# Performance work log

Hardware: AMD Instinct MI355X
Metric: run time of the kernel (lower is better)

## Reference

```python
import jax, jax.numpy as jnp
import numpy as np

N_WIDTH = 8
N_ORDER = 2
N_ELEMENTS = 1024
N_NODES = N_ELEMENTS * N_ORDER + 1  # 2049
N_SAMPLES = 4096
X_MIN = 0.0
X_MAX = 1.0


def _ref_nodes():
    return np.linspace(-1.0, 1.0, N_ORDER + 1)


def _lagrange(x):
    # x: [I, K] -> [I, K, P]
    nodes = _ref_nodes()
    cols = []
    for j in range(N_ORDER + 1):
        p = jnp.ones_like(x)
        for m in range(N_ORDER + 1):
            if j != m:
                p = p * (x - nodes[m]) / (nodes[j] - nodes[m])
        cols.append(p)
    return jnp.stack(cols, axis=-1)


def _dlagrange(x):
    nodes = _ref_nodes()
    cols = []
    for j in range(N_ORDER + 1):
        y = jnp.zeros_like(x)
        for i in range(N_ORDER + 1):
            if i != j:
                k = jnp.ones_like(x) / (nodes[j] - nodes[i])
                for m in range(N_ORDER + 1):
                    if m != i and m != j:
                        k = k * (x - nodes[m]) / (nodes[j] - nodes[m])
                y = y + k
        cols.append(y)
    return jnp.stack(cols, axis=-1)


def _ddlagrange(x):
    nodes = _ref_nodes()
    cols = []
    for j in range(N_ORDER + 1):
        y = jnp.zeros_like(x)
        for i in range(N_ORDER + 1):
            if i != j:
                k_sum = jnp.zeros_like(x)
                for m in range(N_ORDER + 1):
                    if m != i and m != j:
                        k_prod = jnp.ones_like(x) / (nodes[j] - nodes[m])
                        for n in range(N_ORDER + 1):
                            if n != i and n != j and n != m:
                                k_prod = k_prod * (x - nodes[n]) / (nodes[j] - nodes[n])
                        k_sum = k_sum + k_prod
                y = y + (1.0 / (nodes[j] - nodes[i])) * k_sum
        cols.append(y)
    return jnp.stack(cols, axis=-1)


def setup_inputs() -> dict:
    key = jax.random.key(0)
    k1, k2 = jax.random.split(key)
    x = jax.random.uniform(k1, (N_SAMPLES,), dtype=jnp.float32)  # in [x_min, x_max)
    weight = jax.random.normal(k2, (N_WIDTH, N_NODES), dtype=jnp.float32) * 0.02
    return {"x": x, "weight": weight}


def reference(x, weight):
    # replicate 1-D input across width: [I] -> [I, K]
    x2 = jnp.repeat(x[:, None], N_WIDTH, axis=-1)
    x_shift = (N_NODES - 1) * (x2 - X_MIN) / (X_MAX - X_MIN)
    id_el = jnp.clip(jnp.floor(x_shift / N_ORDER), 0, N_ELEMENTS - 1)
    nodes_l = (id_el * N_ORDER).astype(jnp.int32)  # [I, K]
    nodes_lf = jax.lax.stop_gradient(nodes_l.astype(x_shift.dtype))
    # reference coord: (x_shift - 0.5*(l + r)) / (0.5*(r - l)) with r = l + n_order
    x_t = (x_shift - (nodes_lf + 0.5 * N_ORDER)) / (0.5 * N_ORDER)

    delta_x = 0.5 * N_ORDER * (X_MAX - X_MIN) / (N_NODES - 1)
    phi_loc = _lagrange(x_t)                       # [I, K, P]
    dphi_loc = _dlagrange(x_t) / delta_x
    ddphi_loc = _ddlagrange(x_t) / (delta_x * delta_x)

    I, K = x2.shape
    P = N_ORDER + 1
    idx = nodes_l[:, :, None] + jnp.arange(P)      # [I, K, P] global node ids
    ii = jnp.arange(I)[:, None, None]
    kk = jnp.arange(K)[None, :, None]
    phi_ikp = jnp.zeros((I, K, N_NODES), x2.dtype).at[ii, kk, idx].set(phi_loc)
    dphi_ikp = jnp.zeros((I, K, N_NODES), x2.dtype).at[ii, kk, idx].set(dphi_loc)
    ddphi_ikp = jnp.zeros((I, K, N_NODES), x2.dtype).at[ii, kk, idx].set(ddphi_loc)

    t_ik = jnp.einsum('kp,ikp->ik', weight, phi_ikp)
    dt_ik = jnp.einsum('kp,ikp->ik', weight, dphi_ikp)
    ddt_ik = jnp.einsum('kp,ikp->ik', weight, ddphi_ikp)
    return (t_ik, dt_ik, ddt_ik, phi_ikp, dphi_ikp, ddphi_ikp)
```

## Files before the change

### kernel.cpp

```cpp
#include <hip/hip_runtime.h>


#define KN_WIDTH    8
#define KN_ORDER    2
#define KN_ELEMENTS 1024
#define KN_NODES    2049
#define KN_SAMPLES  4096

__global__ __launch_bounds__(256)
void KANN_4578435137547_scatter(const float* __restrict__ x,
                                const float* __restrict__ w,
                                float* __restrict__ out) {
    int i = blockIdx.x * blockDim.x + threadIdx.x;
    if (i >= KN_SAMPLES) return;

    float xv = x[i];
    float x_shift = 2048.0f * xv;
    float fid = floorf(x_shift * 0.5f);
    fid = fminf(fmaxf(fid, 0.0f), (float)(KN_ELEMENTS - 1));
    int nodes_l = (int)fid * KN_ORDER;
    float x_t = x_shift - ((float)nodes_l + 1.0f);

    float phi0 = 0.5f * x_t * (x_t - 1.0f);
    float phi1 = 1.0f - x_t * x_t;
    float phi2 = 0.5f * x_t * (x_t + 1.0f);

    const float inv_dx  = 2048.0f;
    const float inv_dx2 = inv_dx * inv_dx;
    float dphi0 = (x_t - 0.5f) * inv_dx;
    float dphi1 = (-2.0f * x_t) * inv_dx;
    float dphi2 = (x_t + 0.5f) * inv_dx;
    float dd0 =  1.0f * inv_dx2;
    float dd1 = -2.0f * inv_dx2;
    float dd2 =  1.0f * inv_dx2;

    const long long off_dt  = (long long)KN_SAMPLES * KN_WIDTH;
    const long long off_phi = 3LL * KN_SAMPLES * KN_WIDTH;
    const long long sz_phi  = (long long)KN_SAMPLES * KN_WIDTH * KN_NODES;

#pragma unroll
    for (int k = 0; k < KN_WIDTH; ++k) {
        const float* wk = w + k * KN_NODES + nodes_l;
        float w0 = wk[0], w1 = wk[1], w2 = wk[2];
        float t   = w0 * phi0  + w1 * phi1  + w2 * phi2;
        float dt  = w0 * dphi0 + w1 * dphi1 + w2 * dphi2;
        float ddt = w0 * dd0   + w1 * dd1   + w2 * dd2;

        long long ik = (long long)i * KN_WIDTH + k;
        out[ik]              = t;
        out[off_dt + ik]     = dt;
        out[2 * off_dt + ik] = ddt;

        long long base = off_phi + ik * KN_NODES + nodes_l;
        out[base + 0] = phi0;
        out[base + 1] = phi1;
        out[base + 2] = phi2;
        out[base + sz_phi + 0] = dphi0;
        out[base + sz_phi + 1] = dphi1;
        out[base + sz_phi + 2] = dphi2;
        out[base + 2 * sz_phi + 0] = dd0;
        out[base + 2 * sz_phi + 1] = dd1;
        out[base + 2 * sz_phi + 2] = dd2;
    }
}

extern "C" void kernel_launch(void* const* d_in, const int* in_sizes, int n_in,
                              void* d_out, int out_size, void* d_ws, size_t ws_size,
                              hipStream_t stream) {
    const float* x = (const float*)d_in[0];
    const float* w = (const float*)d_in[1];
    float* out = (float*)d_out;

    hipMemsetAsync(out, 0, (size_t)out_size * sizeof(float), stream);

    const int block = 256;
    const int grid = (KN_SAMPLES + block - 1) / block;
    KANN_4578435137547_scatter<<<grid, block, 0, stream>>>(x, w, out);
}
```

Baseline: 158.3 us.

## Replace memset plus scatter with a fused dense float4 writer of basis tensors

Drops the full-output memset and the scattered per-sample stores. A small head kernel now computes t/dt/ddt per (sample, width) thread. A grid-stride body kernel writes each of the three dense basis tensors in one float4-vectorized pass, filling zeros or basis values directly. This turns two passes over roughly 800 MB (clear, then sparse scatter) into one coalesced write stream. The cost is an integer division and a coordinate recompute per float4, plus a slow path for float4s that straddle row boundaries.

```diff
diff --git a/kernel.cpp b/kernel.cpp
--- a/kernel.cpp
+++ b/kernel.cpp
@@ -2,65 +2,86 @@
 
 
 #define KN_WIDTH    8
-#define KN_ORDER    2
-#define KN_ELEMENTS 1024
 #define KN_NODES    2049
 #define KN_SAMPLES  4096
+#define KN_IK       (KN_SAMPLES * KN_WIDTH)
+#define KN_HEAD     (3 * KN_IK)
+#define KN_PHI_LEN  ((size_t)KN_IK * KN_NODES)
+
+__device__ __forceinline__ void kann_coord(float xv, int& nl, float& x_t) {
+    float xs  = 2048.0f * xv;
+    float fid = floorf(0.5f * xs);
+    fid = fminf(fmaxf(fid, 0.0f), 1023.0f);
+    nl  = 2 * (int)fid;
+    x_t = xs - ((float)nl + 1.0f);
+}
 
 __global__ __launch_bounds__(256)
-void KANN_4578435137547_scatter(const float* __restrict__ x,
-                                const float* __restrict__ w,
-                                float* __restrict__ out) {
-    int i = blockIdx.x * blockDim.x + threadIdx.x;
-    if (i >= KN_SAMPLES) return;
+void KANN_head(const float* __restrict__ x, const float* __restrict__ w,
+               float* __restrict__ out) {
+    int ik = blockIdx.x * 256 + threadIdx.x;
+    if (ik >= KN_IK) return;
+    int i = ik >> 3, k = ik & 7;
+    int nl; float x_t; kann_coord(x[i], nl, x_t);
+    float p0 = 0.5f * x_t * (x_t - 1.0f);
+    float p1 = 1.0f - x_t * x_t;
+    float p2 = 0.5f * x_t * (x_t + 1.0f);
+    const float s = 2048.0f, s2 = 2048.0f * 2048.0f;
+    const float* wk = w + k * KN_NODES + nl;
+    float w0 = wk[0], w1 = wk[1], w2 = wk[2];
+    out[ik]             = w0 * p0 + w1 * p1 + w2 * p2;
+    out[KN_IK + ik]     = (w0 * (x_t - 0.5f) - 2.0f * w1 * x_t + w2 * (x_t + 0.5f)) * s;
+    out[2 * KN_IK + ik] = (w0 - 2.0f * w1 + w2) * s2;
+}
 
-    float xv = x[i];
-    float x_shift = 2048.0f * xv;
-    float fid = floorf(x_shift * 0.5f);
-    fid = fminf(fmaxf(fid, 0.0f), (float)(KN_ELEMENTS - 1));
-    int nodes_l = (int)fid * KN_ORDER;
-    float x_t = x_shift - ((float)nodes_l + 1.0f);
+__global__ __launch_bounds__(256)
+void KANN_body(const float* __restrict__ x, float* __restrict__ out) {
+    const int y = blockIdx.y;
+    float* base = out + KN_HEAD + (size_t)y * KN_PHI_LEN;
+    const unsigned nf4 = (unsigned)(KN_PHI_LEN / 4);
+    const unsigned stride = gridDim.x * blockDim.x;
 
-    float phi0 = 0.5f * x_t * (x_t - 1.0f);
-    float phi1 = 1.0f - x_t * x_t;
-    float phi2 = 0.5f * x_t * (x_t + 1.0f);
+    for (unsigned f4 = blockIdx.x * blockDim.x + threadIdx.x; f4 < nf4; f4 += stride) {
+        unsigned e0   = f4 * 4u;
+        unsigned row  = e0 / KN_NODES;
+        unsigned col0 = e0 - row * KN_NODES;
+        float vv[4] = {0.0f, 0.0f, 0.0f, 0.0f};
 
-    const float inv_dx  = 2048.0f;
-    const float inv_dx2 = inv_dx * inv_dx;
-    float dphi0 = (x_t - 0.5f) * inv_dx;
-    float dphi1 = (-2.0f * x_t) * inv_dx;
-    float dphi2 = (x_t + 0.5f) * inv_dx;
-    float dd0 =  1.0f * inv_dx2;
-    float dd1 = -2.0f * inv_dx2;
-    float dd2 =  1.0f * inv_dx2;
-
-    const long long off_dt  = (long long)KN_SAMPLES * KN_WIDTH;
-    const long long off_phi = 3LL * KN_SAMPLES * KN_WIDTH;
-    const long long sz_phi  = (long long)KN_SAMPLES * KN_WIDTH * KN_NODES;
-
+        if (col0 < KN_NODES - 3) {
+            int i = (int)(row >> 3);
+            int nl; float x_t; kann_coord(x[i], nl, x_t);
+            int d0 = (int)col0 - nl;
+            if (d0 >= -3 && d0 <= 2) {
+                float b0, b1, b2;
+                if (y == 0)      { b0 = 0.5f * x_t * (x_t - 1.0f); b1 = 1.0f - x_t * x_t; b2 = 0.5f * x_t * (x_t + 1.0f); }
+                else if (y == 1) { b0 = (x_t - 0.5f) * 2048.0f; b1 = -4096.0f * x_t; b2 = (x_t + 0.5f) * 2048.0f; }
+                else             { b0 = 4194304.0f; b1 = -8388608.0f; b2 = 4194304.0f; }
 #pragma unroll
-    for (int k = 0; k < KN_WIDTH; ++k) {
-        const float* wk = w + k * KN_NODES + nodes_l;
-        float w0 = wk[0], w1 = wk[1], w2 = wk[2];
-        float t   = w0 * phi0  + w1 * phi1  + w2 * phi2;
-        float dt  = w0 * dphi0 + w1 * dphi1 + w2 * dphi2;
-        float ddt = w0 * dd0   + w1 * dd1   + w2 * dd2;
-
-        long long ik = (long long)i * KN_WIDTH + k;
-        out[ik]              = t;
-        out[off_dt + ik]     = dt;
-        out[2 * off_dt + ik] = ddt;
-
-        long long base = off_phi + ik * KN_NODES + nodes_l;
-        out[base + 0] = phi0;
-        out[base + 1] = phi1;
-        out[base + 2] = phi2;
-        out[base + sz_phi + 0] = dphi0;
-        out[base + sz_phi + 1] = dphi1;
-        out[base + sz_phi + 2] = dphi2;
-        out[base + 2 * sz_phi + 0] = dd0;
-        out[base + 2 * sz_phi + 1] = dd1;
-        out[base + 2 * sz_phi + 2] = dd2;
+                for (int j = 0; j < 4; ++j) {
+                    int d = d0 + j;
+                    vv[j] = (d == 0) ? b0 : ((d == 1) ? b1 : ((d == 2) ? b2 : 0.0f));
+                }
+            }
+        } else {
+#pragma unroll
+            for (int j = 0; j < 4; ++j) {
+                unsigned e = e0 + j;
+                unsigned r = e / KN_NODES;
+                unsigned c = e - r * KN_NODES;
+                int i = (int)(r >> 3);
+                int nl; float x_t; kann_coord(x[i], nl, x_t);
+                int d = (int)c - nl;
+                if (d >= 0 && d <= 2) {
+                    float b;
+                    if (y == 0)      b = (d == 0) ? 0.5f * x_t * (x_t - 1.0f) : ((d == 1) ? 1.0f - x_t * x_t : 0.5f * x_t * (x_t + 1.0f));
+                    else if (y == 1) b = ((d == 0) ? (x_t - 0.5f) : ((d == 1) ? (-2.0f * x_t) : (x_t + 0.5f))) * 2048.0f;
+                    else             b = (d == 1) ? -8388608.0f : 4194304.0f;
+                    vv[j] = b;
+                }
+            }
+        }
+        float4 v = make_float4(vv[0], vv[1], vv[2], vv[3]);
+        *reinterpret_cast<float4*>(base + (size_t)e0) = v;
     }
 }
 
@@ -71,9 +92,6 @@
     const float* w = (const float*)d_in[1];
     float* out = (float*)d_out;
 
-    hipMemsetAsync(out, 0, (size_t)out_size * sizeof(float), stream);
-
-    const int block = 256;
-    const int grid = (KN_SAMPLES + block - 1) / block;
-    KANN_4578435137547_scatter<<<grid, block, 0, stream>>>(x, w, out);
+    KANN_head<<<dim3(KN_IK / 256), dim3(256), 0, stream>>>(x, w, out);
+    KANN_body<<<dim3(1024, 3), dim3(256), 0, stream>>>(x, out);
 }
```

Result: slower. 161.7 us (+2.2%).
